# Performance work log

Hardware: AMD Instinct MI355X
Metric: run time of the kernel (lower is better)

## Reference

```python
import jax, jax.numpy as jnp
import numpy as np

N, E, HDIM, NG = 10000, 320000, 256, 20
BN_EPS = 1e-5


def setup_inputs() -> dict:
    key = jax.random.key(0)
    ks = jax.random.split(key, 12)
    inp = {
        "x": jax.random.normal(ks[0], (N, HDIM), dtype=jnp.float32),
        "rbf": jax.random.uniform(ks[1], (E, NG), dtype=jnp.float32),
        "ei": jax.random.randint(ks[2], (2, E), 0, N, dtype=jnp.int64),
        # filter_net: Linear(n_g, hdim) -> SiLU -> Linear(hdim, hdim)
        "Wf1": jax.random.normal(ks[3], (NG, HDIM), dtype=jnp.float32) / np.sqrt(NG),
        "bf1": jnp.zeros((HDIM,), dtype=jnp.float32),
        "Wf2": jax.random.normal(ks[4], (HDIM, HDIM), dtype=jnp.float32) / np.sqrt(HDIM),
        "bf2": jnp.zeros((HDIM,), dtype=jnp.float32),
        # node_update: Linear(hdim, hdim) -> SiLU -> Linear(hdim, hdim)
        "Wu1": jax.random.normal(ks[5], (HDIM, HDIM), dtype=jnp.float32) / np.sqrt(HDIM),
        "bu1": jnp.zeros((HDIM,), dtype=jnp.float32),
        "Wu2": jax.random.normal(ks[6], (HDIM, HDIM), dtype=jnp.float32) / np.sqrt(HDIM),
        "bu2": jnp.zeros((HDIM,), dtype=jnp.float32),
        # BatchNorm1d affine params
        "gamma": jnp.ones((HDIM,), dtype=jnp.float32),
        "beta": jnp.zeros((HDIM,), dtype=jnp.float32),
    }
    return inp


def reference(x, rbf, Wf1, bf1, Wf2, bf2, Wu1, bu1, Wu2, bu2, gamma, beta, ei):
    row, col = ei[0], ei[1]
    # filter_net(rbf): [E, hdim]
    filt = jax.nn.silu(rbf @ Wf1 + bf1) @ Wf2 + bf2
    # message = gather(x, col) * filter
    msg = x[col] * filt  # [E, hdim]
    # scatter_add aggregation over destination nodes
    agg = jax.ops.segment_sum(msg, row, num_segments=x.shape[0])  # [N, hdim]
    # node_update MLP
    h = jax.nn.silu(agg @ Wu1 + bu1) @ Wu2 + bu2  # [N, hdim]
    # BatchNorm1d (training mode: batch stats, biased variance)
    mean = jnp.mean(h, axis=0)
    var = jnp.mean(jnp.square(h - mean), axis=0)
    bn = gamma * (h - mean) * jax.lax.rsqrt(var + BN_EPS) + beta
    return x + bn
```

## Files before the change

### kernel.cpp

```cpp
#include <hip/hip_runtime.h>

#define N_NODES 10000
#define E_EDGES 320000
#define HDIM    256
#define NG      20
#define BN_EPS  1e-5f

typedef __attribute__((ext_vector_type(8))) short short8;
typedef __attribute__((ext_vector_type(4))) float f32x4;

__device__ __forceinline__ float silu_f(float v) {
    float e = __expf(-v);
    return v * __builtin_amdgcn_rcpf(1.0f + e);
}

__device__ __forceinline__ unsigned int cvt_pk(float lo, float hi) {
    unsigned int r;
    asm("v_cvt_pk_bf16_f32 %0, %1, %2" : "=v"(r) : "v"(lo), "v"(hi));
    return r;
}

__device__ __forceinline__ unsigned short f2bf(float f) {
    union { float f; unsigned int u; } v; v.f = f;
    unsigned int r = v.u + 0x7fffu + ((v.u >> 16) & 1u);
    return (unsigned short)(r >> 16);
}

__global__ __launch_bounds__(256) void prep_kernel(
    const float* __restrict__ Wf2, const float* __restrict__ Wu1,
    const float* __restrict__ Wu2, const float* __restrict__ Wf1,
    const float* __restrict__ bf1,
    unsigned short* __restrict__ Pf2, unsigned short* __restrict__ Pu1,
    unsigned short* __restrict__ Pu2, unsigned short* __restrict__ P1)
{
    if (blockIdx.y == 3) {
        if (blockIdx.x >= 32) return;
        int tid = blockIdx.x * 256 + threadIdx.x;
        int j     = tid & 7;
        int lane  = (tid >> 3) & 63;
        int ntile = tid >> 9;
        int k = (lane >> 4) * 8 + j;
        int n = ntile * 16 + (lane & 15);
        float v = (k < NG) ? Wf1[k * 256 + n] : (k == NG ? bf1[n] : 0.0f);
        P1[tid] = f2bf(v);
        return;
    }
    const float* W = (blockIdx.y == 0) ? Wf2 : (blockIdx.y == 1) ? Wu1 : Wu2;
    unsigned short* P = (blockIdx.y == 0) ? Pf2 : (blockIdx.y == 1) ? Pu1 : Pu2;
    int tid   = blockIdx.x * 256 + threadIdx.x;
    int j     = tid & 7;
    int lane  = (tid >> 3) & 63;
    int ntile = (tid >> 9) & 15;
    int kstep = tid >> 13;
    int k = kstep * 32 + (lane >> 4) * 8 + j;
    int n = ntile * 16 + (lane & 15);
    P[tid] = f2bf(W[k * 256 + n]);
}

__global__ __launch_bounds__(256) void hist_kernel(const int* __restrict__ ei_row,
                                                   int* __restrict__ cnt) {
    int e = blockIdx.x * 256 + threadIdx.x;
    atomicAdd(&cnt[ei_row[e]], 1);
}

__global__ __launch_bounds__(256) void scan_kernel(int* __restrict__ cnt) {
    __shared__ int tot[256];
    const int t = threadIdx.x;
    int loc[40];
    int s = 0;
    #pragma unroll
    for (int i = 0; i < 40; ++i) { loc[i] = cnt[t * 40 + i]; s += loc[i]; }
    tot[t] = s;
    __syncthreads();
    for (int off = 1; off < 256; off <<= 1) {
        int u = (t >= off) ? tot[t - off] : 0;
        __syncthreads();
        tot[t] += u;
        __syncthreads();
    }
    int pre = tot[t] - s;
    #pragma unroll
    for (int i = 0; i < 40; ++i) { int v = loc[i]; cnt[t * 40 + i] = pre; pre += v; }
}

__global__ __launch_bounds__(256) void fill_kernel(const int* __restrict__ ei_row,
                                                   int* __restrict__ cnt,
                                                   int* __restrict__ perm,
                                                   int* __restrict__ nodepos) {
    int e = blockIdx.x * 256 + threadIdx.x;
    int r = ei_row[e];
    int pos = atomicAdd(&cnt[r], 1);
    perm[pos] = e;
    nodepos[pos] = r;
}

#define SM_NID 0
#define SM_COL 256
#define SM_RBF 512
#define SM_HID 4608
#define SM_TOT 37376

__global__ __launch_bounds__(256, 3) void edge_kernel(
    const float* __restrict__ rbf, const int* __restrict__ ei_col,
    const int* __restrict__ perm, const int* __restrict__ nodepos,
    const unsigned short* __restrict__ P1, const unsigned short* __restrict__ P2,
    const float* __restrict__ bf2, const float* __restrict__ x,
    float* __restrict__ agg)
{
    __shared__ char sm[SM_TOT];
    int* nid_s = (int*)(sm + SM_NID);
    int* col_s = (int*)(sm + SM_COL);

    const int t = threadIdx.x;
    int blk = blockIdx.x;
    blk = (blk & 7) * (E_EDGES / 64 / 8) + (blk >> 3);
    const int p0 = blk * 64;
    const int l = t & 63, w = t >> 6;
    const int l15 = l & 15, l4 = l >> 4;

    if (t < 64) {
        nid_s[t] = nodepos[p0 + t];
        col_s[t] = ei_col[perm[p0 + t]];
    }
    if (t < 128) {
        const int row = t >> 1, half = t & 1;
        const float* rp = rbf + (size_t)perm[p0 + row] * NG + half * 10;
        float v[10];
        if (half == 0) {
            float4 a = *(const float4*)rp, b = *(const float4*)(rp + 4);
            float2 c = *(const float2*)(rp + 8);
            v[0]=a.x; v[1]=a.y; v[2]=a.z; v[3]=a.w; v[4]=b.x;
            v[5]=b.y; v[6]=b.z; v[7]=b.w; v[8]=c.x; v[9]=c.y;
        } else {
            float2 a = *(const float2*)rp;
            float4 b = *(const float4*)(rp + 2), c = *(const float4*)(rp + 6);
            v[0]=a.x; v[1]=a.y; v[2]=b.x; v[3]=b.y; v[4]=b.z;
            v[5]=b.w; v[6]=c.x; v[7]=c.y; v[8]=c.z; v[9]=c.w;
        }
        unsigned int* dst = (unsigned int*)(sm + SM_RBF + row * 64 + half * 20);
        #pragma unroll
        for (int i = 0; i < 5; ++i) dst[i] = cvt_pk(v[2*i], v[2*i+1]);
    } else if (t < 192) {
        const int row = t - 128;
        *(unsigned long long*)(sm + SM_RBF + row * 64 + 40) = 0x3F80ull;
        *(uint4*)(sm + SM_RBF + row * 64 + 48) = make_uint4(0, 0, 0, 0);
    }

    short8 a1[4], acur[4];
    #pragma unroll
    for (int mt = 0; mt < 4; ++mt) {
        a1[mt]   = *(const short8*)(P1 + ((4 * w + mt) * 64 + l) * 8);
        acur[mt] = *(const short8*)(P2 + ((4 * w + mt) * 64 + l) * 8);
    }

    __syncthreads();

    f32x4 acc[4][4];
    #pragma unroll
    for (int mt = 0; mt < 4; ++mt)
        #pragma unroll
        for (int nt = 0; nt < 4; ++nt) acc[mt][nt] = (f32x4)0.0f;

    #pragma unroll
    for (int nt = 0; nt < 4; ++nt) {
        short8 bfr = *(const short8*)(sm + SM_RBF + (nt * 16 + l15) * 64 + l4 * 16);
        #pragma unroll
        for (int mt = 0; mt < 4; ++mt)
            acc[mt][nt] = __builtin_amdgcn_mfma_f32_16x16x32_bf16(a1[mt], bfr, acc[mt][nt], 0, 0, 0);
    }

    #pragma unroll
    for (int mt = 0; mt < 4; ++mt) {
        const int hc0 = w * 64 + mt * 16 + l4 * 4;
        #pragma unroll
        for (int nt = 0; nt < 4; ++nt) {
            const int row = nt * 16 + l15;
            unsigned int pk0 = cvt_pk(silu_f(acc[mt][nt][0]), silu_f(acc[mt][nt][1]));
            unsigned int pk1 = cvt_pk(silu_f(acc[mt][nt][2]), silu_f(acc[mt][nt][3]));
            *(uint2*)(sm + SM_HID + row * 512 +
                      (((hc0 >> 3) ^ (row & 7)) << 4) + (hc0 & 7) * 2) =
                make_uint2(pk0, pk1);
        }
    }
    __syncthreads();

    #pragma unroll
    for (int mt = 0; mt < 4; ++mt)
        #pragma unroll
        for (int nt = 0; nt < 4; ++nt) acc[mt][nt] = (f32x4)0.0f;

    for (int ks = 0; ks < 8; ++ks) {
        short8 anext[4];
        if (ks < 7) {
            #pragma unroll
            for (int mt = 0; mt < 4; ++mt)
                anext[mt] = *(const short8*)(P2 + (((ks + 1) * 16 + 4 * w + mt) * 64 + l) * 8);
        }
        #pragma unroll
        for (int nt = 0; nt < 4; ++nt) {
            const int row = nt * 16 + l15;
            short8 bfh = *(const short8*)(sm + SM_HID + row * 512 +
                            ((((ks << 2) + l4) ^ (row & 7)) << 4));
            #pragma unroll
            for (int mt = 0; mt < 4; ++mt)
                acc[mt][nt] = __builtin_amdgcn_mfma_f32_16x16x32_bf16(acur[mt], bfh, acc[mt][nt], 0, 0, 0);
        }
        if (ks < 7) {
            #pragma unroll
            for (int mt = 0; mt < 4; ++mt) acur[mt] = anext[mt];
        }
    }
    __syncthreads();

    f32x4 bc4[4];
    #pragma unroll
    for (int mt = 0; mt < 4; ++mt)
        bc4[mt] = *(const f32x4*)(bf2 + w * 64 + mt * 16 + l4 * 4);

    const float* xbase[4];
    #pragma unroll
    for (int nt = 0; nt < 4; ++nt)
        xbase[nt] = x + (size_t)col_s[nt * 16 + l15] * HDIM;

    float sum = 0.0f;
    int cur = nid_s[0];

    #pragma unroll
    for (int ms = 0; ms < 2; ++ms) {
        #pragma unroll
        for (int ni = 0; ni < 2; ++ni) {
            const int nt  = ms * 2 + ni;
            const int pos = ni * 16 + l15;
            #pragma unroll
            for (int mt = 0; mt < 4; ++mt) {
                const int fc0 = w * 64 + mt * 16 + l4 * 4;
                f32x4 xv = *(const f32x4*)(xbase[nt] + fc0);
                f32x4 mv = (acc[mt][nt] + bc4[mt]) * xv;
                *(f32x4*)(sm + SM_HID + pos * 1024 +
                          (((fc0 >> 2) ^ (pos & 7)) << 4)) = mv;
            }
        }
        __syncthreads();
        for (int pos = 0; pos < 32; ++pos) {
            const int row = ms * 32 + pos;
            const int nid = nid_s[row];
            float v = *(const float*)(sm + SM_HID + pos * 1024 +
                        (((t >> 2) ^ (pos & 7)) << 4) + (t & 3) * 4);
            if (nid != cur) {
                atomicAdd(&agg[(size_t)cur * HDIM + t], sum);
                sum = 0.0f; cur = nid;
            }
            sum += v;
        }
        __syncthreads();
    }
    atomicAdd(&agg[(size_t)cur * HDIM + t], sum);
}

__global__ __launch_bounds__(256, 3) void node_kernel(
    const float* __restrict__ agg, const float* __restrict__ bu1,
    const float* __restrict__ bu2,
    const unsigned short* __restrict__ Pu1, const unsigned short* __restrict__ Pu2,
    float* __restrict__ hout, float* __restrict__ sums)
{
    __shared__ char sm[32768];
    const int t  = threadIdx.x;
    const int r0 = blockIdx.x * 64;
    const int l = t & 63, w = t >> 6;
    const int l15 = l & 15, l4 = l >> 4;

    {
        const int row = t & 63, q = t >> 6;
        const bool valid = (r0 + row) < N_NODES;
        const float4* src = (const float4*)(agg + (size_t)(r0 + row) * HDIM) + q * 16;
        #pragma unroll
        for (int i = 0; i < 16; ++i) {
            float4 v = valid ? src[i] : make_float4(0.f, 0.f, 0.f, 0.f);
            const int c0 = q * 64 + i * 4;
            *(uint2*)(sm + row * 512 + (((c0 >> 3) ^ (row & 7)) << 4) + (c0 & 7) * 2) =
                make_uint2(cvt_pk(v.x, v.y), cvt_pk(v.z, v.w));
        }
    }

    short8 acur[4];
    #pragma unroll
    for (int mt = 0; mt < 4; ++mt)
        acur[mt] = *(const short8*)(Pu1 + ((4 * w + mt) * 64 + l) * 8);

    __syncthreads();

    f32x4 acc[4][4];
    #pragma unroll
    for (int mt = 0; mt < 4; ++mt)
        #pragma unroll
        for (int nt = 0; nt < 4; ++nt) acc[mt][nt] = (f32x4)0.0f;

    for (int ks = 0; ks < 8; ++ks) {
        short8 anext[4];
        if (ks < 7) {
            #pragma unroll
            for (int mt = 0; mt < 4; ++mt)
                anext[mt] = *(const short8*)(Pu1 + (((ks + 1) * 16 + 4 * w + mt) * 64 + l) * 8);
        }
        #pragma unroll
        for (int nt = 0; nt < 4; ++nt) {
            const int row = nt * 16 + l15;
            short8 bfa = *(const short8*)(sm + row * 512 +
                            ((((ks << 2) + l4) ^ (row & 7)) << 4));
            #pragma unroll
            for (int mt = 0; mt < 4; ++mt)
                acc[mt][nt] = __builtin_amdgcn_mfma_f32_16x16x32_bf16(acur[mt], bfa, acc[mt][nt], 0, 0, 0);
        }
        if (ks < 7) {
            #pragma unroll
            for (int mt = 0; mt < 4; ++mt) acur[mt] = anext[mt];
        }
    }
    __syncthreads();

    #pragma unroll
    for (int mt = 0; mt < 4; ++mt)
        acur[mt] = *(const short8*)(Pu2 + ((4 * w + mt) * 64 + l) * 8);

    #pragma unroll
    for (int mt = 0; mt < 4; ++mt) {
        const int mc0 = w * 64 + mt * 16 + l4 * 4;
        f32x4 b4 = *(const f32x4*)(bu1 + mc0);
        #pragma unroll
        for (int nt = 0; nt < 4; ++nt) {
            const int row = nt * 16 + l15;
            unsigned int pk0 = cvt_pk(silu_f(acc[mt][nt][0] + b4[0]), silu_f(acc[mt][nt][1] + b4[1]));
            unsigned int pk1 = cvt_pk(silu_f(acc[mt][nt][2] + b4[2]), silu_f(acc[mt][nt][3] + b4[3]));
            *(uint2*)(sm + row * 512 + (((mc0 >> 3) ^ (row & 7)) << 4) + (mc0 & 7) * 2) =
                make_uint2(pk0, pk1);
            acc[mt][nt] = (f32x4)0.0f;
        }
    }
    __syncthreads();

    for (int ks = 0; ks < 8; ++ks) {
        short8 anext[4];
        if (ks < 7) {
            #pragma unroll
            for (int mt = 0; mt < 4; ++mt)
                anext[mt] = *(const short8*)(Pu2 + (((ks + 1) * 16 + 4 * w + mt) * 64 + l) * 8);
        }
        #pragma unroll
        for (int nt = 0; nt < 4; ++nt) {
            const int row = nt * 16 + l15;
            short8 bfm = *(const short8*)(sm + row * 512 +
                            ((((ks << 2) + l4) ^ (row & 7)) << 4));
            #pragma unroll
            for (int mt = 0; mt < 4; ++mt)
                acc[mt][nt] = __builtin_amdgcn_mfma_f32_16x16x32_bf16(acur[mt], bfm, acc[mt][nt], 0, 0, 0);
        }
        if (ks < 7) {
            #pragma unroll
            for (int mt = 0; mt < 4; ++mt) acur[mt] = anext[mt];
        }
    }

    #pragma unroll
    for (int mt = 0; mt < 4; ++mt) {
        const int hc0 = w * 64 + mt * 16 + l4 * 4;
        f32x4 b4 = *(const f32x4*)(bu2 + hc0);
        f32x4 s = (f32x4)0.0f, s2 = (f32x4)0.0f;
        #pragma unroll
        for (int nt = 0; nt < 4; ++nt) {
            const int gr = r0 + nt * 16 + l15;
            if (gr < N_NODES) {
                f32x4 hv = acc[mt][nt] + b4;
                *(f32x4*)(hout + (size_t)gr * HDIM + hc0) = hv;
                s += hv; s2 += hv * hv;
            }
        }
        #pragma unroll
        for (int off = 1; off < 16; off <<= 1) {
            #pragma unroll
            for (int r = 0; r < 4; ++r) {
                s[r]  += __shfl_xor(s[r], off);
                s2[r] += __shfl_xor(s2[r], off);
            }
        }
        if (l15 == 0) {
            #pragma unroll
            for (int r = 0; r < 4; ++r) {
                atomicAdd(&sums[hc0 + r], s[r]);
                atomicAdd(&sums[HDIM + hc0 + r], s2[r]);
            }
        }
    }
}

__global__ __launch_bounds__(256) void final_kernel(
    const float* __restrict__ x, const float* __restrict__ sums,
    const float* __restrict__ gamma, const float* __restrict__ beta,
    float* __restrict__ out)
{
    const int i = blockIdx.x * 256 + threadIdx.x;
    const int j = i & (HDIM - 1);
    const float mean = sums[j] * (1.0f / N_NODES);
    const float var  = sums[HDIM + j] * (1.0f / N_NODES) - mean * mean;
    const float inv  = rsqrtf(var + BN_EPS);
    const float hv   = out[i];
    out[i] = x[i] + gamma[j] * (hv - mean) * inv + beta[j];
}

extern "C" void kernel_launch(void* const* d_in, const int* in_sizes, int n_in,
                              void* d_out, int out_size, void* d_ws, size_t ws_size,
                              hipStream_t stream) {
    const float* x     = (const float*)d_in[0];
    const float* rbf   = (const float*)d_in[1];
    const int*   ei    = (const int*)d_in[2];
    const float* Wf1   = (const float*)d_in[3];
    const float* bf1   = (const float*)d_in[4];
    const float* Wf2   = (const float*)d_in[5];
    const float* bf2   = (const float*)d_in[6];
    const float* Wu1   = (const float*)d_in[7];
    const float* bu1   = (const float*)d_in[8];
    const float* Wu2   = (const float*)d_in[9];
    const float* bu2   = (const float*)d_in[10];
    const float* gamma = (const float*)d_in[11];
    const float* beta  = (const float*)d_in[12];
    float* out = (float*)d_out;

    char* ws = (char*)d_ws;
    float* agg     = (float*)(ws);
    float* sums    = (float*)(ws + 10240000);
    int*   cnt     = (int*)(ws + 10242048);
    int*   perm    = (int*)(ws + 10283008);
    int*   nodepos = (int*)(ws + 11563008);
    unsigned short* Pf2 = (unsigned short*)(ws + 12843008);
    unsigned short* Pu1 = (unsigned short*)(ws + 12974080);
    unsigned short* Pu2 = (unsigned short*)(ws + 13105152);
    unsigned short* P1  = (unsigned short*)(ws + 13236224);

    hipMemsetAsync(agg, 0, 10283008, stream);

    prep_kernel<<<dim3(256, 4), 256, 0, stream>>>(Wf2, Wu1, Wu2, Wf1, bf1,
                                                  Pf2, Pu1, Pu2, P1);
    hist_kernel<<<E_EDGES / 256, 256, 0, stream>>>(ei, cnt);
    scan_kernel<<<1, 256, 0, stream>>>(cnt);
    fill_kernel<<<E_EDGES / 256, 256, 0, stream>>>(ei, cnt, perm, nodepos);

    edge_kernel<<<E_EDGES / 64, 256, 0, stream>>>(
        rbf, ei + E_EDGES, perm, nodepos, P1, Pf2, bf2, x, agg);
    node_kernel<<<(N_NODES + 63) / 64, 256, 0, stream>>>(
        agg, bu1, bu2, Pu1, Pu2, out, sums);
    final_kernel<<<(N_NODES * HDIM) / 256, 256, 0, stream>>>(x, sums, gamma, beta, out);
}
```

Baseline: 205.5 us.

## Enlarge edge tiles, fuse prep with histogram, shrink node tiles, vectorize final kernel

The edge kernel now processes 128 edges per 512-thread block. Each wave reads rbf directly from global memory into MFMA operands instead of staging it in LDS, and segmented reduction is split between two halves of the block. The weight-packing kernel is merged with the histogram kernel to remove a launch. The node kernel uses 32-row tiles for more blocks and higher occupancy, and the final BN kernel is vectorized to float4. Trade-offs: 64KB LDS per edge block limits residency, there are more atomics per tile boundary, and weight reuse per node block is lower.

```diff
diff --git a/kernel.cpp b/kernel.cpp
--- a/kernel.cpp
+++ b/kernel.cpp
@@ -5,9 +5,12 @@
 #define HDIM    256
 #define NG      20
 #define BN_EPS  1e-5f
+#define EB      128
+#define RB      32
 
 typedef __attribute__((ext_vector_type(8))) short short8;
 typedef __attribute__((ext_vector_type(4))) float f32x4;
+typedef __attribute__((ext_vector_type(4))) unsigned int u32x4;
 
 __device__ __forceinline__ float silu_f(float v) {
     float e = __expf(-v);
@@ -26,41 +29,45 @@
     return (unsigned short)(r >> 16);
 }
 
-__global__ __launch_bounds__(256) void prep_kernel(
+__device__ __forceinline__ short8 mk_s8(unsigned int a, unsigned int b,
+                                        unsigned int c, unsigned int d) {
+    union { u32x4 u; short8 s; } v;
+    v.u = (u32x4){a, b, c, d};
+    return v.s;
+}
+
+__global__ __launch_bounds__(256) void prep_hist_kernel(
     const float* __restrict__ Wf2, const float* __restrict__ Wu1,
     const float* __restrict__ Wu2, const float* __restrict__ Wf1,
-    const float* __restrict__ bf1,
+    const float* __restrict__ bf1, const int* __restrict__ ei_row,
     unsigned short* __restrict__ Pf2, unsigned short* __restrict__ Pu1,
-    unsigned short* __restrict__ Pu2, unsigned short* __restrict__ P1)
+    unsigned short* __restrict__ Pu2, unsigned short* __restrict__ P1,
+    int* __restrict__ cnt)
 {
-    if (blockIdx.y == 3) {
-        if (blockIdx.x >= 32) return;
-        int tid = blockIdx.x * 256 + threadIdx.x;
-        int j     = tid & 7;
-        int lane  = (tid >> 3) & 63;
-        int ntile = tid >> 9;
+    const int bx = blockIdx.x;
+    if (bx >= 800) {
+        int e = (bx - 800) * 256 + threadIdx.x;
+        atomicAdd(&cnt[ei_row[e]], 1);
+        return;
+    }
+    int tid = bx * 256 + threadIdx.x;
+    if (tid < 196608) {
+        int which = tid >> 16, local = tid & 65535;
+        const float* W = (which == 0) ? Wf2 : (which == 1) ? Wu1 : Wu2;
+        unsigned short* P = (which == 0) ? Pf2 : (which == 1) ? Pu1 : Pu2;
+        int j = local & 7, lane = (local >> 3) & 63;
+        int ntile = (local >> 9) & 15, kstep = local >> 13;
+        int k = kstep * 32 + (lane >> 4) * 8 + j;
+        int n = ntile * 16 + (lane & 15);
+        P[local] = f2bf(W[k * 256 + n]);
+    } else {
+        int local = tid - 196608;
+        int j = local & 7, lane = (local >> 3) & 63, ntile = local >> 9;
         int k = (lane >> 4) * 8 + j;
         int n = ntile * 16 + (lane & 15);
         float v = (k < NG) ? Wf1[k * 256 + n] : (k == NG ? bf1[n] : 0.0f);
-        P1[tid] = f2bf(v);
-        return;
-    }
-    const float* W = (blockIdx.y == 0) ? Wf2 : (blockIdx.y == 1) ? Wu1 : Wu2;
-    unsigned short* P = (blockIdx.y == 0) ? Pf2 : (blockIdx.y == 1) ? Pu1 : Pu2;
-    int tid   = blockIdx.x * 256 + threadIdx.x;
-    int j     = tid & 7;
-    int lane  = (tid >> 3) & 63;
-    int ntile = (tid >> 9) & 15;
-    int kstep = tid >> 13;
-    int k = kstep * 32 + (lane >> 4) * 8 + j;
-    int n = ntile * 16 + (lane & 15);
-    P[tid] = f2bf(W[k * 256 + n]);
-}
-
-__global__ __launch_bounds__(256) void hist_kernel(const int* __restrict__ ei_row,
-                                                   int* __restrict__ cnt) {
-    int e = blockIdx.x * 256 + threadIdx.x;
-    atomicAdd(&cnt[ei_row[e]], 1);
+        P1[local] = f2bf(v);
+    }
 }
 
 __global__ __launch_bounds__(256) void scan_kernel(int* __restrict__ cnt) {
@@ -94,76 +101,63 @@
     nodepos[pos] = r;
 }
 
-#define SM_NID 0
-#define SM_COL 256
-#define SM_RBF 512
-#define SM_HID 4608
-#define SM_TOT 37376
-
-__global__ __launch_bounds__(256, 3) void edge_kernel(
+__global__ __launch_bounds__(512, 4) void edge_kernel(
     const float* __restrict__ rbf, const int* __restrict__ ei_col,
     const int* __restrict__ perm, const int* __restrict__ nodepos,
     const unsigned short* __restrict__ P1, const unsigned short* __restrict__ P2,
     const float* __restrict__ bf2, const float* __restrict__ x,
     float* __restrict__ agg)
 {
-    __shared__ char sm[SM_TOT];
-    int* nid_s = (int*)(sm + SM_NID);
-    int* col_s = (int*)(sm + SM_COL);
+    __shared__ char sm[65536];
 
     const int t = threadIdx.x;
     int blk = blockIdx.x;
-    blk = (blk & 7) * (E_EDGES / 64 / 8) + (blk >> 3);
-    const int p0 = blk * 64;
+    {
+        int xcd = blk & 7, i = blk >> 3;
+        blk = (xcd < 4 ? xcd * 313 : 1252 + (xcd - 4) * 312) + i;
+    }
+    const int p0 = blk * EB;
     const int l = t & 63, w = t >> 6;
+    const int wq = w & 3, wh = w >> 2;
     const int l15 = l & 15, l4 = l >> 4;
 
-    if (t < 64) {
-        nid_s[t] = nodepos[p0 + t];
-        col_s[t] = ei_col[perm[p0 + t]];
-    }
-    if (t < 128) {
-        const int row = t >> 1, half = t & 1;
-        const float* rp = rbf + (size_t)perm[p0 + row] * NG + half * 10;
-        float v[10];
-        if (half == 0) {
-            float4 a = *(const float4*)rp, b = *(const float4*)(rp + 4);
-            float2 c = *(const float2*)(rp + 8);
-            v[0]=a.x; v[1]=a.y; v[2]=a.z; v[3]=a.w; v[4]=b.x;
-            v[5]=b.y; v[6]=b.z; v[7]=b.w; v[8]=c.x; v[9]=c.y;
+    int rowsl[4], ecol[4];
+    const float* rbfp[4];
+    #pragma unroll
+    for (int nt = 0; nt < 4; ++nt) {
+        int row = wh * 64 + nt * 16 + l15;
+        rowsl[nt] = row;
+        int e = perm[p0 + row];
+        ecol[nt] = ei_col[e];
+        rbfp[nt] = rbf + (size_t)e * NG;
+    }
+
+    short8 a1[4];
+    #pragma unroll
+    for (int mt = 0; mt < 4; ++mt)
+        a1[mt] = *(const short8*)(P1 + ((4 * wq + mt) * 64 + l) * 8);
+
+    f32x4 acc[4][4];
+    #pragma unroll
+    for (int mt = 0; mt < 4; ++mt)
+        #pragma unroll
+        for (int nt = 0; nt < 4; ++nt) acc[mt][nt] = (f32x4)0.0f;
+
+    #pragma unroll
+    for (int nt = 0; nt < 4; ++nt) {
+        short8 bfr;
+        if (l4 < 2) {
+            float4 fa = *(const float4*)(rbfp[nt] + l4 * 8);
+            float4 fb = *(const float4*)(rbfp[nt] + l4 * 8 + 4);
+            bfr = mk_s8(cvt_pk(fa.x, fa.y), cvt_pk(fa.z, fa.w),
+                        cvt_pk(fb.x, fb.y), cvt_pk(fb.z, fb.w));
+        } else if (l4 == 2) {
+            float4 fa = *(const float4*)(rbfp[nt] + 16);
+            bfr = mk_s8(cvt_pk(fa.x, fa.y), cvt_pk(fa.z, fa.w),
+                        0x00003f80u , 0u);
         } else {
-            float2 a = *(const float2*)rp;
-            float4 b = *(const float4*)(rp + 2), c = *(const float4*)(rp + 6);
-            v[0]=a.x; v[1]=a.y; v[2]=b.x; v[3]=b.y; v[4]=b.z;
-            v[5]=b.w; v[6]=c.x; v[7]=c.y; v[8]=c.z; v[9]=c.w;
-        }
-        unsigned int* dst = (unsigned int*)(sm + SM_RBF + row * 64 + half * 20);
-        #pragma unroll
-        for (int i = 0; i < 5; ++i) dst[i] = cvt_pk(v[2*i], v[2*i+1]);
-    } else if (t < 192) {
-        const int row = t - 128;
-        *(unsigned long long*)(sm + SM_RBF + row * 64 + 40) = 0x3F80ull;
-        *(uint4*)(sm + SM_RBF + row * 64 + 48) = make_uint4(0, 0, 0, 0);
-    }
-
-    short8 a1[4], acur[4];
-    #pragma unroll
-    for (int mt = 0; mt < 4; ++mt) {
-        a1[mt]   = *(const short8*)(P1 + ((4 * w + mt) * 64 + l) * 8);
-        acur[mt] = *(const short8*)(P2 + ((4 * w + mt) * 64 + l) * 8);
-    }
-
-    __syncthreads();
-
-    f32x4 acc[4][4];
-    #pragma unroll
-    for (int mt = 0; mt < 4; ++mt)
-        #pragma unroll
-        for (int nt = 0; nt < 4; ++nt) acc[mt][nt] = (f32x4)0.0f;
-
-    #pragma unroll
-    for (int nt = 0; nt < 4; ++nt) {
-        short8 bfr = *(const short8*)(sm + SM_RBF + (nt * 16 + l15) * 64 + l4 * 16);
+            bfr = mk_s8(0u, 0u, 0u, 0u);
+        }
         #pragma unroll
         for (int mt = 0; mt < 4; ++mt)
             acc[mt][nt] = __builtin_amdgcn_mfma_f32_16x16x32_bf16(a1[mt], bfr, acc[mt][nt], 0, 0, 0);
@@ -171,17 +165,22 @@
 
     #pragma unroll
     for (int mt = 0; mt < 4; ++mt) {
-        const int hc0 = w * 64 + mt * 16 + l4 * 4;
+        const int hc0 = wq * 64 + mt * 16 + l4 * 4;
         #pragma unroll
         for (int nt = 0; nt < 4; ++nt) {
-            const int row = nt * 16 + l15;
+            const int row = rowsl[nt];
             unsigned int pk0 = cvt_pk(silu_f(acc[mt][nt][0]), silu_f(acc[mt][nt][1]));
             unsigned int pk1 = cvt_pk(silu_f(acc[mt][nt][2]), silu_f(acc[mt][nt][3]));
-            *(uint2*)(sm + SM_HID + row * 512 +
-                      (((hc0 >> 3) ^ (row & 7)) << 4) + (hc0 & 7) * 2) =
+            *(uint2*)(sm + row * 512 + (((hc0 >> 3) ^ (row & 7)) << 4) + (hc0 & 7) * 2) =
                 make_uint2(pk0, pk1);
         }
     }
+
+    short8 acur[4];
+    #pragma unroll
+    for (int mt = 0; mt < 4; ++mt)
+        acur[mt] = *(const short8*)(P2 + ((4 * wq + mt) * 64 + l) * 8);
+
     __syncthreads();
 
     #pragma unroll
@@ -194,12 +193,12 @@
         if (ks < 7) {
             #pragma unroll
             for (int mt = 0; mt < 4; ++mt)
-                anext[mt] = *(const short8*)(P2 + (((ks + 1) * 16 + 4 * w + mt) * 64 + l) * 8);
+                anext[mt] = *(const short8*)(P2 + (((ks + 1) * 16 + 4 * wq + mt) * 64 + l) * 8);
         }
         #pragma unroll
         for (int nt = 0; nt < 4; ++nt) {
-            const int row = nt * 16 + l15;
-            short8 bfh = *(const short8*)(sm + SM_HID + row * 512 +
+            const int row = rowsl[nt];
+            short8 bfh = *(const short8*)(sm + row * 512 +
                             ((((ks << 2) + l4) ^ (row & 7)) << 4));
             #pragma unroll
             for (int mt = 0; mt < 4; ++mt)
@@ -215,68 +214,70 @@
     f32x4 bc4[4];
     #pragma unroll
     for (int mt = 0; mt < 4; ++mt)
-        bc4[mt] = *(const f32x4*)(bf2 + w * 64 + mt * 16 + l4 * 4);
-
-    const float* xbase[4];
-    #pragma unroll
-    for (int nt = 0; nt < 4; ++nt)
-        xbase[nt] = x + (size_t)col_s[nt * 16 + l15] * HDIM;
-
-    float sum = 0.0f;
-    int cur = nid_s[0];
-
-    #pragma unroll
-    for (int ms = 0; ms < 2; ++ms) {
-        #pragma unroll
-        for (int ni = 0; ni < 2; ++ni) {
-            const int nt  = ms * 2 + ni;
-            const int pos = ni * 16 + l15;
-            #pragma unroll
-            for (int mt = 0; mt < 4; ++mt) {
-                const int fc0 = w * 64 + mt * 16 + l4 * 4;
-                f32x4 xv = *(const f32x4*)(xbase[nt] + fc0);
-                f32x4 mv = (acc[mt][nt] + bc4[mt]) * xv;
-                *(f32x4*)(sm + SM_HID + pos * 1024 +
-                          (((fc0 >> 2) ^ (pos & 7)) << 4)) = mv;
+        bc4[mt] = *(const f32x4*)(bf2 + wq * 64 + mt * 16 + l4 * 4);
+
+    const int rcol = t & 255;
+    const int rh   = t >> 8;
+
+    #pragma unroll
+    for (int ps = 0; ps < 2; ++ps) {
+        if (wh == ps) {
+            #pragma unroll
+            for (int nt = 0; nt < 4; ++nt) {
+                const int lrow = nt * 16 + l15;
+                const float* xp = x + (size_t)ecol[nt] * HDIM;
+                #pragma unroll
+                for (int mt = 0; mt < 4; ++mt) {
+                    const int fc0 = wq * 64 + mt * 16 + l4 * 4;
+                    f32x4 xv = *(const f32x4*)(xp + fc0);
+                    f32x4 mv = (acc[mt][nt] + bc4[mt]) * xv;
+                    *(f32x4*)(sm + lrow * 1024 + (((fc0 >> 2) ^ (lrow & 7)) << 4)) = mv;
+                }
             }
         }
         __syncthreads();
-        for (int pos = 0; pos < 32; ++pos) {
-            const int row = ms * 32 + pos;
-            const int nid = nid_s[row];
-            float v = *(const float*)(sm + SM_HID + pos * 1024 +
-                        (((t >> 2) ^ (pos & 7)) << 4) + (t & 3) * 4);
-            if (nid != cur) {
-                atomicAdd(&agg[(size_t)cur * HDIM + t], sum);
-                sum = 0.0f; cur = nid;
+        {
+            const int base = p0 + ps * 64 + rh * 32;
+            float sum = 0.0f;
+            int cur = nodepos[base];
+            #pragma unroll 8
+            for (int pos = 0; pos < 32; ++pos) {
+                const int lrow = rh * 32 + pos;
+                const int nid = nodepos[base + pos];
+                float v = *(const float*)(sm + lrow * 1024 +
+                            (((rcol >> 2) ^ (lrow & 7)) << 4) + (rcol & 3) * 4);
+                if (nid != cur) {
+                    atomicAdd(&agg[(size_t)cur * HDIM + rcol], sum);
+                    sum = 0.0f; cur = nid;
+                }
+                sum += v;
             }
-            sum += v;
+            atomicAdd(&agg[(size_t)cur * HDIM + rcol], sum);
         }
         __syncthreads();
     }
-    atomicAdd(&agg[(size_t)cur * HDIM + t], sum);
-}
-
-__global__ __launch_bounds__(256, 3) void node_kernel(
+}
+
+__global__ __launch_bounds__(256, 4) void node_kernel(
     const float* __restrict__ agg, const float* __restrict__ bu1,
     const float* __restrict__ bu2,
     const unsigned short* __restrict__ Pu1, const unsigned short* __restrict__ Pu2,
     float* __restrict__ hout, float* __restrict__ sums)
 {
-    __shared__ char sm[32768];
+    __shared__ char sm[16384];
     const int t  = threadIdx.x;
-    const int r0 = blockIdx.x * 64;
+    const int r0 = blockIdx.x * RB;
     const int l = t & 63, w = t >> 6;
     const int l15 = l & 15, l4 = l >> 4;
 
     {
-        const int row = t & 63, q = t >> 6;
+        const int row = t & 31, q = t >> 5;
         const bool valid = (r0 + row) < N_NODES;
-        const float4* src = (const float4*)(agg + (size_t)(r0 + row) * HDIM) + q * 16;
-        #pragma unroll
-        for (int i = 0; i < 16; ++i) {
+        const float4* src = (const float4*)(agg + (size_t)(r0 + row) * HDIM) + q * 8;
+        #pragma unroll
+        for (int i = 0; i < 8; ++i) {
             float4 v = valid ? src[i] : make_float4(0.f, 0.f, 0.f, 0.f);
-            const int c0 = q * 64 + i * 4;
+            const int c0 = q * 32 + i * 4;
             *(uint2*)(sm + row * 512 + (((c0 >> 3) ^ (row & 7)) << 4) + (c0 & 7) * 2) =
                 make_uint2(cvt_pk(v.x, v.y), cvt_pk(v.z, v.w));
         }
@@ -289,11 +290,11 @@
 
     __syncthreads();
 
-    f32x4 acc[4][4];
-    #pragma unroll
-    for (int mt = 0; mt < 4; ++mt)
-        #pragma unroll
-        for (int nt = 0; nt < 4; ++nt) acc[mt][nt] = (f32x4)0.0f;
+    f32x4 acc[4][2];
+    #pragma unroll
+    for (int mt = 0; mt < 4; ++mt)
+        #pragma unroll
+        for (int nt = 0; nt < 2; ++nt) acc[mt][nt] = (f32x4)0.0f;
 
     for (int ks = 0; ks < 8; ++ks) {
         short8 anext[4];
@@ -303,7 +304,7 @@
                 anext[mt] = *(const short8*)(Pu1 + (((ks + 1) * 16 + 4 * w + mt) * 64 + l) * 8);
         }
         #pragma unroll
-        for (int nt = 0; nt < 4; ++nt) {
+        for (int nt = 0; nt < 2; ++nt) {
             const int row = nt * 16 + l15;
             short8 bfa = *(const short8*)(sm + row * 512 +
                             ((((ks << 2) + l4) ^ (row & 7)) << 4));
@@ -327,7 +328,7 @@
         const int mc0 = w * 64 + mt * 16 + l4 * 4;
         f32x4 b4 = *(const f32x4*)(bu1 + mc0);
         #pragma unroll
-        for (int nt = 0; nt < 4; ++nt) {
+        for (int nt = 0; nt < 2; ++nt) {
             const int row = nt * 16 + l15;
             unsigned int pk0 = cvt_pk(silu_f(acc[mt][nt][0] + b4[0]), silu_f(acc[mt][nt][1] + b4[1]));
             unsigned int pk1 = cvt_pk(silu_f(acc[mt][nt][2] + b4[2]), silu_f(acc[mt][nt][3] + b4[3]));
@@ -346,7 +347,7 @@
                 anext[mt] = *(const short8*)(Pu2 + (((ks + 1) * 16 + 4 * w + mt) * 64 + l) * 8);
         }
         #pragma unroll
-        for (int nt = 0; nt < 4; ++nt) {
+        for (int nt = 0; nt < 2; ++nt) {
             const int row = nt * 16 + l15;
             short8 bfm = *(const short8*)(sm + row * 512 +
                             ((((ks << 2) + l4) ^ (row & 7)) << 4));
@@ -366,7 +367,7 @@
         f32x4 b4 = *(const f32x4*)(bu2 + hc0);
         f32x4 s = (f32x4)0.0f, s2 = (f32x4)0.0f;
         #pragma unroll
-        for (int nt = 0; nt < 4; ++nt) {
+        for (int nt = 0; nt < 2; ++nt) {
             const int gr = r0 + nt * 16 + l15;
             if (gr < N_NODES) {
                 f32x4 hv = acc[mt][nt] + b4;
@@ -397,13 +398,19 @@
     const float* __restrict__ gamma, const float* __restrict__ beta,
     float* __restrict__ out)
 {
-    const int i = blockIdx.x * 256 + threadIdx.x;
-    const int j = i & (HDIM - 1);
-    const float mean = sums[j] * (1.0f / N_NODES);
-    const float var  = sums[HDIM + j] * (1.0f / N_NODES) - mean * mean;
-    const float inv  = rsqrtf(var + BN_EPS);
-    const float hv   = out[i];
-    out[i] = x[i] + gamma[j] * (hv - mean) * inv + beta[j];
+    const int i4 = blockIdx.x * 256 + threadIdx.x;
+    const int j  = (i4 & 63) * 4;
+    f32x4 mean = *(const f32x4*)(sums + j) * (1.0f / N_NODES);
+    f32x4 s2   = *(const f32x4*)(sums + HDIM + j) * (1.0f / N_NODES);
+    f32x4 g    = *(const f32x4*)(gamma + j);
+    f32x4 b    = *(const f32x4*)(beta + j);
+    f32x4 hv   = ((f32x4*)out)[i4];
+    f32x4 xv   = ((const f32x4*)x)[i4];
+    f32x4 var  = s2 - mean * mean;
+    f32x4 inv;
+    #pragma unroll
+    for (int r = 0; r < 4; ++r) inv[r] = rsqrtf(var[r] + BN_EPS);
+    ((f32x4*)out)[i4] = xv + g * (hv - mean) * inv + b;
 }
 
 extern "C" void kernel_launch(void* const* d_in, const int* in_sizes, int n_in,
@@ -437,15 +444,15 @@
 
     hipMemsetAsync(agg, 0, 10283008, stream);
 
-    prep_kernel<<<dim3(256, 4), 256, 0, stream>>>(Wf2, Wu1, Wu2, Wf1, bf1,
-                                                  Pf2, Pu1, Pu2, P1);
-    hist_kernel<<<E_EDGES / 256, 256, 0, stream>>>(ei, cnt);
+    prep_hist_kernel<<<2050, 256, 0, stream>>>(Wf2, Wu1, Wu2, Wf1, bf1, ei,
+                                               Pf2, Pu1, Pu2, P1, cnt);
     scan_kernel<<<1, 256, 0, stream>>>(cnt);
     fill_kernel<<<E_EDGES / 256, 256, 0, stream>>>(ei, cnt, perm, nodepos);
 
-    edge_kernel<<<E_EDGES / 64, 256, 0, stream>>>(
+    edge_kernel<<<E_EDGES / EB, 512, 0, stream>>>(
         rbf, ei + E_EDGES, perm, nodepos, P1, Pf2, bf2, x, agg);
-    node_kernel<<<(N_NODES + 63) / 64, 256, 0, stream>>>(
+    node_kernel<<<(N_NODES + RB - 1) / RB, 256, 0, stream>>>(
         agg, bu1, bu2, Pu1, Pu2, out, sums);
-    final_kernel<<<(N_NODES * HDIM) / 256, 256, 0, stream>>>(x, sums, gamma, beta, out);
-}
+    final_kernel<<<(N_NODES * HDIM / 4) / 256, 256, 0, stream>>>(
+        x, sums, gamma, beta, out);
+}
```

Result: slower. 307.3 us (+49.5%).

## Merge prep/hist kernels, prefetch x gathers, shrink node tiles, vectorize final

Applied to the files above, without the earlier changes.

Fuses weight packing and the edge-row histogram into one launch. In the edge kernel, x-row gathers are prefetched during the second GEMM and overlapped with the scatter phase, and the RBF smem row stride is padded to 80 bytes to reduce bank conflicts. The node kernel now uses 16-row tiles (625 blocks, less smem, higher occupancy) instead of 64-row tiles, and the final BN kernel is vectorized to float4. Smaller node tiles reload the weight fragments more often and issue more atomics on the stats sums.

```diff
diff --git a/kernel.cpp b/kernel.cpp
--- a/kernel.cpp
+++ b/kernel.cpp
@@ -5,6 +5,7 @@
 #define HDIM    256
 #define NG      20
 #define BN_EPS  1e-5f
+#define RB      16
 
 typedef __attribute__((ext_vector_type(8))) short short8;
 typedef __attribute__((ext_vector_type(4))) float f32x4;
@@ -26,41 +27,38 @@
     return (unsigned short)(r >> 16);
 }
 
-__global__ __launch_bounds__(256) void prep_kernel(
+__global__ __launch_bounds__(256) void prep_hist_kernel(
     const float* __restrict__ Wf2, const float* __restrict__ Wu1,
     const float* __restrict__ Wu2, const float* __restrict__ Wf1,
-    const float* __restrict__ bf1,
+    const float* __restrict__ bf1, const int* __restrict__ ei_row,
     unsigned short* __restrict__ Pf2, unsigned short* __restrict__ Pu1,
-    unsigned short* __restrict__ Pu2, unsigned short* __restrict__ P1)
+    unsigned short* __restrict__ Pu2, unsigned short* __restrict__ P1,
+    int* __restrict__ cnt)
 {
-    if (blockIdx.y == 3) {
-        if (blockIdx.x >= 32) return;
-        int tid = blockIdx.x * 256 + threadIdx.x;
-        int j     = tid & 7;
-        int lane  = (tid >> 3) & 63;
-        int ntile = tid >> 9;
+    const int bx = blockIdx.x;
+    if (bx >= 800) {
+        int e = (bx - 800) * 256 + threadIdx.x;
+        atomicAdd(&cnt[ei_row[e]], 1);
+        return;
+    }
+    int tid = bx * 256 + threadIdx.x;
+    if (tid < 196608) {
+        int which = tid >> 16, local = tid & 65535;
+        const float* W = (which == 0) ? Wf2 : (which == 1) ? Wu1 : Wu2;
+        unsigned short* P = (which == 0) ? Pf2 : (which == 1) ? Pu1 : Pu2;
+        int j = local & 7, lane = (local >> 3) & 63;
+        int ntile = (local >> 9) & 15, kstep = local >> 13;
+        int k = kstep * 32 + (lane >> 4) * 8 + j;
+        int n = ntile * 16 + (lane & 15);
+        P[local] = f2bf(W[k * 256 + n]);
+    } else {
+        int local = tid - 196608;
+        int j = local & 7, lane = (local >> 3) & 63, ntile = local >> 9;
         int k = (lane >> 4) * 8 + j;
         int n = ntile * 16 + (lane & 15);
         float v = (k < NG) ? Wf1[k * 256 + n] : (k == NG ? bf1[n] : 0.0f);
-        P1[tid] = f2bf(v);
-        return;
-    }
-    const float* W = (blockIdx.y == 0) ? Wf2 : (blockIdx.y == 1) ? Wu1 : Wu2;
-    unsigned short* P = (blockIdx.y == 0) ? Pf2 : (blockIdx.y == 1) ? Pu1 : Pu2;
-    int tid   = blockIdx.x * 256 + threadIdx.x;
-    int j     = tid & 7;
-    int lane  = (tid >> 3) & 63;
-    int ntile = (tid >> 9) & 15;
-    int kstep = tid >> 13;
-    int k = kstep * 32 + (lane >> 4) * 8 + j;
-    int n = ntile * 16 + (lane & 15);
-    P[tid] = f2bf(W[k * 256 + n]);
-}
-
-__global__ __launch_bounds__(256) void hist_kernel(const int* __restrict__ ei_row,
-                                                   int* __restrict__ cnt) {
-    int e = blockIdx.x * 256 + threadIdx.x;
-    atomicAdd(&cnt[ei_row[e]], 1);
+        P1[local] = f2bf(v);
+    }
 }
 
 __global__ __launch_bounds__(256) void scan_kernel(int* __restrict__ cnt) {
@@ -97,8 +95,8 @@
 #define SM_NID 0
 #define SM_COL 256
 #define SM_RBF 512
-#define SM_HID 4608
-#define SM_TOT 37376
+#define SM_HID 5632
+#define SM_TOT 38400
 
 __global__ __launch_bounds__(256, 3) void edge_kernel(
     const float* __restrict__ rbf, const int* __restrict__ ei_col,
@@ -113,7 +111,7 @@
 
     const int t = threadIdx.x;
     int blk = blockIdx.x;
-    blk = (blk & 7) * (E_EDGES / 64 / 8) + (blk >> 3);
+    blk = (blk & 7) * 625 + (blk >> 3);
     const int p0 = blk * 64;
     const int l = t & 63, w = t >> 6;
     const int l15 = l & 15, l4 = l >> 4;
@@ -137,13 +135,13 @@
             v[0]=a.x; v[1]=a.y; v[2]=b.x; v[3]=b.y; v[4]=b.z;
             v[5]=b.w; v[6]=c.x; v[7]=c.y; v[8]=c.z; v[9]=c.w;
         }
-        unsigned int* dst = (unsigned int*)(sm + SM_RBF + row * 64 + half * 20);
+        unsigned int* dst = (unsigned int*)(sm + SM_RBF + row * 80 + half * 20);
         #pragma unroll
         for (int i = 0; i < 5; ++i) dst[i] = cvt_pk(v[2*i], v[2*i+1]);
     } else if (t < 192) {
         const int row = t - 128;
-        *(unsigned long long*)(sm + SM_RBF + row * 64 + 40) = 0x3F80ull;
-        *(uint4*)(sm + SM_RBF + row * 64 + 48) = make_uint4(0, 0, 0, 0);
+        *(unsigned long long*)(sm + SM_RBF + row * 80 + 40) = 0x3F80ull;
+        *(uint4*)(sm + SM_RBF + row * 80 + 48) = make_uint4(0, 0, 0, 0);
     }
 
     short8 a1[4], acur[4];
@@ -155,6 +153,11 @@
 
     __syncthreads();
 
+    const float* xbase[4];
+    #pragma unroll
+    for (int nt = 0; nt < 4; ++nt)
+        xbase[nt] = x + (size_t)col_s[nt * 16 + l15] * HDIM;
+
     f32x4 acc[4][4];
     #pragma unroll
     for (int mt = 0; mt < 4; ++mt)
@@ -163,7 +166,7 @@
 
     #pragma unroll
     for (int nt = 0; nt < 4; ++nt) {
-        short8 bfr = *(const short8*)(sm + SM_RBF + (nt * 16 + l15) * 64 + l4 * 16);
+        short8 bfr = *(const short8*)(sm + SM_RBF + (nt * 16 + l15) * 80 + l4 * 16);
         #pragma unroll
         for (int mt = 0; mt < 4; ++mt)
             acc[mt][nt] = __builtin_amdgcn_mfma_f32_16x16x32_bf16(a1[mt], bfr, acc[mt][nt], 0, 0, 0);
@@ -189,12 +192,22 @@
         #pragma unroll
         for (int nt = 0; nt < 4; ++nt) acc[mt][nt] = (f32x4)0.0f;
 
+    f32x4 xp[8];
+
     for (int ks = 0; ks < 8; ++ks) {
         short8 anext[4];
         if (ks < 7) {
             #pragma unroll
             for (int mt = 0; mt < 4; ++mt)
                 anext[mt] = *(const short8*)(P2 + (((ks + 1) * 16 + 4 * w + mt) * 64 + l) * 8);
+        }
+        if (ks == 6) {
+            #pragma unroll
+            for (int mt = 0; mt < 4; ++mt) {
+                const int fc0 = w * 64 + mt * 16 + l4 * 4;
+                xp[mt]     = *(const f32x4*)(xbase[0] + fc0);
+                xp[4 + mt] = *(const f32x4*)(xbase[1] + fc0);
+            }
         }
         #pragma unroll
         for (int nt = 0; nt < 4; ++nt) {
@@ -217,66 +230,83 @@
     for (int mt = 0; mt < 4; ++mt)
         bc4[mt] = *(const f32x4*)(bf2 + w * 64 + mt * 16 + l4 * 4);
 
-    const float* xbase[4];
-    #pragma unroll
-    for (int nt = 0; nt < 4; ++nt)
-        xbase[nt] = x + (size_t)col_s[nt * 16 + l15] * HDIM;
-
     float sum = 0.0f;
     int cur = nid_s[0];
 
     #pragma unroll
-    for (int ms = 0; ms < 2; ++ms) {
-        #pragma unroll
-        for (int ni = 0; ni < 2; ++ni) {
-            const int nt  = ms * 2 + ni;
-            const int pos = ni * 16 + l15;
-            #pragma unroll
-            for (int mt = 0; mt < 4; ++mt) {
-                const int fc0 = w * 64 + mt * 16 + l4 * 4;
-                f32x4 xv = *(const f32x4*)(xbase[nt] + fc0);
-                f32x4 mv = (acc[mt][nt] + bc4[mt]) * xv;
-                *(f32x4*)(sm + SM_HID + pos * 1024 +
-                          (((fc0 >> 2) ^ (pos & 7)) << 4)) = mv;
-            }
-        }
-        __syncthreads();
-        for (int pos = 0; pos < 32; ++pos) {
-            const int row = ms * 32 + pos;
-            const int nid = nid_s[row];
-            float v = *(const float*)(sm + SM_HID + pos * 1024 +
-                        (((t >> 2) ^ (pos & 7)) << 4) + (t & 3) * 4);
-            if (nid != cur) {
-                atomicAdd(&agg[(size_t)cur * HDIM + t], sum);
-                sum = 0.0f; cur = nid;
-            }
-            sum += v;
-        }
-        __syncthreads();
+    for (int ni = 0; ni < 2; ++ni) {
+        const int nt  = ni;
+        const int pos = ni * 16 + l15;
+        #pragma unroll
+        for (int mt = 0; mt < 4; ++mt) {
+            const int fc0 = w * 64 + mt * 16 + l4 * 4;
+            f32x4 mv = (acc[mt][nt] + bc4[mt]) * xp[ni * 4 + mt];
+            *(f32x4*)(sm + SM_HID + pos * 1024 + (((fc0 >> 2) ^ (pos & 7)) << 4)) = mv;
+        }
+    }
+    #pragma unroll
+    for (int mt = 0; mt < 4; ++mt) {
+        const int fc0 = w * 64 + mt * 16 + l4 * 4;
+        xp[mt]     = *(const f32x4*)(xbase[2] + fc0);
+        xp[4 + mt] = *(const f32x4*)(xbase[3] + fc0);
+    }
+    __syncthreads();
+    for (int pos = 0; pos < 32; ++pos) {
+        const int nid = nid_s[pos];
+        float v = *(const float*)(sm + SM_HID + pos * 1024 +
+                    (((t >> 2) ^ (pos & 7)) << 4) + (t & 3) * 4);
+        if (nid != cur) {
+            atomicAdd(&agg[(size_t)cur * HDIM + t], sum);
+            sum = 0.0f; cur = nid;
+        }
+        sum += v;
+    }
+    __syncthreads();
+
+    #pragma unroll
+    for (int ni = 0; ni < 2; ++ni) {
+        const int nt  = 2 + ni;
+        const int pos = ni * 16 + l15;
+        #pragma unroll
+        for (int mt = 0; mt < 4; ++mt) {
+            const int fc0 = w * 64 + mt * 16 + l4 * 4;
+            f32x4 mv = (acc[mt][nt] + bc4[mt]) * xp[ni * 4 + mt];
+            *(f32x4*)(sm + SM_HID + pos * 1024 + (((fc0 >> 2) ^ (pos & 7)) << 4)) = mv;
+        }
+    }
+    __syncthreads();
+    for (int pos = 0; pos < 32; ++pos) {
+        const int nid = nid_s[32 + pos];
+        float v = *(const float*)(sm + SM_HID + pos * 1024 +
+                    (((t >> 2) ^ (pos & 7)) << 4) + (t & 3) * 4);
+        if (nid != cur) {
+            atomicAdd(&agg[(size_t)cur * HDIM + t], sum);
+            sum = 0.0f; cur = nid;
+        }
+        sum += v;
     }
     atomicAdd(&agg[(size_t)cur * HDIM + t], sum);
 }
 
-__global__ __launch_bounds__(256, 3) void node_kernel(
+__global__ __launch_bounds__(256, 4) void node_kernel(
     const float* __restrict__ agg, const float* __restrict__ bu1,
     const float* __restrict__ bu2,
     const unsigned short* __restrict__ Pu1, const unsigned short* __restrict__ Pu2,
     float* __restrict__ hout, float* __restrict__ sums)
 {
-    __shared__ char sm[32768];
+    __shared__ char sm[8192];
     const int t  = threadIdx.x;
-    const int r0 = blockIdx.x * 64;
+    const int r0 = blockIdx.x * RB;
     const int l = t & 63, w = t >> 6;
     const int l15 = l & 15, l4 = l >> 4;
 
     {
-        const int row = t & 63, q = t >> 6;
-        const bool valid = (r0 + row) < N_NODES;
-        const float4* src = (const float4*)(agg + (size_t)(r0 + row) * HDIM) + q * 16;
-        #pragma unroll
-        for (int i = 0; i < 16; ++i) {
-            float4 v = valid ? src[i] : make_float4(0.f, 0.f, 0.f, 0.f);
-            const int c0 = q * 64 + i * 4;
+        const int row = t & 15, q = t >> 4;
+        const float4* src = (const float4*)(agg + (size_t)(r0 + row) * HDIM) + q * 4;
+        #pragma unroll
+        for (int i = 0; i < 4; ++i) {
+            float4 v = src[i];
+            const int c0 = q * 16 + i * 4;
             *(uint2*)(sm + row * 512 + (((c0 >> 3) ^ (row & 7)) << 4) + (c0 & 7) * 2) =
                 make_uint2(cvt_pk(v.x, v.y), cvt_pk(v.z, v.w));
         }
@@ -289,11 +319,9 @@
 
     __syncthreads();
 
-    f32x4 acc[4][4];
-    #pragma unroll
-    for (int mt = 0; mt < 4; ++mt)
-        #pragma unroll
-        for (int nt = 0; nt < 4; ++nt) acc[mt][nt] = (f32x4)0.0f;
+    f32x4 acc[4];
+    #pragma unroll
+    for (int mt = 0; mt < 4; ++mt) acc[mt] = (f32x4)0.0f;
 
     for (int ks = 0; ks < 8; ++ks) {
         short8 anext[4];
@@ -302,15 +330,11 @@
             for (int mt = 0; mt < 4; ++mt)
                 anext[mt] = *(const short8*)(Pu1 + (((ks + 1) * 16 + 4 * w + mt) * 64 + l) * 8);
         }
-        #pragma unroll
-        for (int nt = 0; nt < 4; ++nt) {
-            const int row = nt * 16 + l15;
-            short8 bfa = *(const short8*)(sm + row * 512 +
-                            ((((ks << 2) + l4) ^ (row & 7)) << 4));
-            #pragma unroll
-            for (int mt = 0; mt < 4; ++mt)
-                acc[mt][nt] = __builtin_amdgcn_mfma_f32_16x16x32_bf16(acur[mt], bfa, acc[mt][nt], 0, 0, 0);
-        }
+        short8 bfa = *(const short8*)(sm + l15 * 512 +
+                        ((((ks << 2) + l4) ^ (l15 & 7)) << 4));
+        #pragma unroll
+        for (int mt = 0; mt < 4; ++mt)
+            acc[mt] = __builtin_amdgcn_mfma_f32_16x16x32_bf16(acur[mt], bfa, acc[mt], 0, 0, 0);
         if (ks < 7) {
             #pragma unroll
             for (int mt = 0; mt < 4; ++mt) acur[mt] = anext[mt];
@@ -326,15 +350,11 @@
     for (int mt = 0; mt < 4; ++mt) {
         const int mc0 = w * 64 + mt * 16 + l4 * 4;
         f32x4 b4 = *(const f32x4*)(bu1 + mc0);
-        #pragma unroll
-        for (int nt = 0; nt < 4; ++nt) {
-            const int row = nt * 16 + l15;
-            unsigned int pk0 = cvt_pk(silu_f(acc[mt][nt][0] + b4[0]), silu_f(acc[mt][nt][1] + b4[1]));
-            unsigned int pk1 = cvt_pk(silu_f(acc[mt][nt][2] + b4[2]), silu_f(acc[mt][nt][3] + b4[3]));
-            *(uint2*)(sm + row * 512 + (((mc0 >> 3) ^ (row & 7)) << 4) + (mc0 & 7) * 2) =
-                make_uint2(pk0, pk1);
-            acc[mt][nt] = (f32x4)0.0f;
-        }
+        unsigned int pk0 = cvt_pk(silu_f(acc[mt][0] + b4[0]), silu_f(acc[mt][1] + b4[1]));
+        unsigned int pk1 = cvt_pk(silu_f(acc[mt][2] + b4[2]), silu_f(acc[mt][3] + b4[3]));
+        *(uint2*)(sm + l15 * 512 + (((mc0 >> 3) ^ (l15 & 7)) << 4) + (mc0 & 7) * 2) =
+            make_uint2(pk0, pk1);
+        acc[mt] = (f32x4)0.0f;
     }
     __syncthreads();
 
@@ -345,15 +365,11 @@
             for (int mt = 0; mt < 4; ++mt)
                 anext[mt] = *(const short8*)(Pu2 + (((ks + 1) * 16 + 4 * w + mt) * 64 + l) * 8);
         }
-        #pragma unroll
-        for (int nt = 0; nt < 4; ++nt) {
-            const int row = nt * 16 + l15;
-            short8 bfm = *(const short8*)(sm + row * 512 +
-                            ((((ks << 2) + l4) ^ (row & 7)) << 4));
-            #pragma unroll
-            for (int mt = 0; mt < 4; ++mt)
-                acc[mt][nt] = __builtin_amdgcn_mfma_f32_16x16x32_bf16(acur[mt], bfm, acc[mt][nt], 0, 0, 0);
-        }
+        short8 bfm = *(const short8*)(sm + l15 * 512 +
+                        ((((ks << 2) + l4) ^ (l15 & 7)) << 4));
+        #pragma unroll
+        for (int mt = 0; mt < 4; ++mt)
+            acc[mt] = __builtin_amdgcn_mfma_f32_16x16x32_bf16(acur[mt], bfm, acc[mt], 0, 0, 0);
         if (ks < 7) {
             #pragma unroll
             for (int mt = 0; mt < 4; ++mt) acur[mt] = anext[mt];
@@ -364,16 +380,10 @@
     for (int mt = 0; mt < 4; ++mt) {
         const int hc0 = w * 64 + mt * 16 + l4 * 4;
         f32x4 b4 = *(const f32x4*)(bu2 + hc0);
-        f32x4 s = (f32x4)0.0f, s2 = (f32x4)0.0f;
-        #pragma unroll
-        for (int nt = 0; nt < 4; ++nt) {
-            const int gr = r0 + nt * 16 + l15;
-            if (gr < N_NODES) {
-                f32x4 hv = acc[mt][nt] + b4;
-                *(f32x4*)(hout + (size_t)gr * HDIM + hc0) = hv;
-                s += hv; s2 += hv * hv;
-            }
-        }
+        const int gr = r0 + l15;
+        f32x4 hv = acc[mt] + b4;
+        *(f32x4*)(hout + (size_t)gr * HDIM + hc0) = hv;
+        f32x4 s = hv, s2 = hv * hv;
         #pragma unroll
         for (int off = 1; off < 16; off <<= 1) {
             #pragma unroll
@@ -397,13 +407,19 @@
     const float* __restrict__ gamma, const float* __restrict__ beta,
     float* __restrict__ out)
 {
-    const int i = blockIdx.x * 256 + threadIdx.x;
-    const int j = i & (HDIM - 1);
-    const float mean = sums[j] * (1.0f / N_NODES);
-    const float var  = sums[HDIM + j] * (1.0f / N_NODES) - mean * mean;
-    const float inv  = rsqrtf(var + BN_EPS);
-    const float hv   = out[i];
-    out[i] = x[i] + gamma[j] * (hv - mean) * inv + beta[j];
+    const int i4 = blockIdx.x * 256 + threadIdx.x;
+    const int j  = (i4 & 63) * 4;
+    f32x4 mean = *(const f32x4*)(sums + j) * (1.0f / N_NODES);
+    f32x4 s2   = *(const f32x4*)(sums + HDIM + j) * (1.0f / N_NODES);
+    f32x4 g    = *(const f32x4*)(gamma + j);
+    f32x4 b    = *(const f32x4*)(beta + j);
+    f32x4 hv   = ((f32x4*)out)[i4];
+    f32x4 xv   = ((const f32x4*)x)[i4];
+    f32x4 var  = s2 - mean * mean;
+    f32x4 inv;
+    #pragma unroll
+    for (int r = 0; r < 4; ++r) inv[r] = rsqrtf(var[r] + BN_EPS);
+    ((f32x4*)out)[i4] = xv + g * (hv - mean) * inv + b;
 }
 
 extern "C" void kernel_launch(void* const* d_in, const int* in_sizes, int n_in,
@@ -437,15 +453,15 @@
 
     hipMemsetAsync(agg, 0, 10283008, stream);
 
-    prep_kernel<<<dim3(256, 4), 256, 0, stream>>>(Wf2, Wu1, Wu2, Wf1, bf1,
-                                                  Pf2, Pu1, Pu2, P1);
-    hist_kernel<<<E_EDGES / 256, 256, 0, stream>>>(ei, cnt);
+    prep_hist_kernel<<<2050, 256, 0, stream>>>(Wf2, Wu1, Wu2, Wf1, bf1, ei,
+                                               Pf2, Pu1, Pu2, P1, cnt);
     scan_kernel<<<1, 256, 0, stream>>>(cnt);
     fill_kernel<<<E_EDGES / 256, 256, 0, stream>>>(ei, cnt, perm, nodepos);
 
     edge_kernel<<<E_EDGES / 64, 256, 0, stream>>>(
         rbf, ei + E_EDGES, perm, nodepos, P1, Pf2, bf2, x, agg);
-    node_kernel<<<(N_NODES + 63) / 64, 256, 0, stream>>>(
+    node_kernel<<<N_NODES / RB, 256, 0, stream>>>(
         agg, bu1, bu2, Pu1, Pu2, out, sums);
-    final_kernel<<<(N_NODES * HDIM) / 256, 256, 0, stream>>>(x, sums, gamma, beta, out);
-}
+    final_kernel<<<(N_NODES * HDIM / 4) / 256, 256, 0, stream>>>(
+        x, sums, gamma, beta, out);
+}
```

After: 244.1 us. 18.8% more time.
